# Performance work log

Hardware: AMD Instinct MI355X
Metric: run time of the kernel (lower is better)

The kernel has to match this reference:

```python
import jax, jax.numpy as jnp
import numpy as np

B, H, W = 512, 36, 36
N = H * W          # 1296 oscillators
K = 8              # couplings per oscillator
EP0 = 0.1          # kura_update_rate
ANNEAL = 0.5


def setup_inputs() -> dict:
    key = jax.random.key(0)
    k = jax.random.split(key, 8)
    return {
        "input": jax.random.normal(k[0], (B, H, W), jnp.float32),
        "initial_phase": jax.random.uniform(k[1], (B, N), jnp.float32) * (2.0 * np.pi),
        "connectivity": jax.random.randint(k[2], (B, N, K), 0, N),
        "episodes": 25,
        "conv1_w": jax.random.normal(k[3], (8, 1, 3, 3), jnp.float32) * 0.1,
        "conv1_b": jnp.zeros((8,), jnp.float32),
        "conv2_w": jax.random.normal(k[4], (16, 8, 3, 3), jnp.float32) * 0.1,
        "conv2_b": jnp.zeros((16,), jnp.float32),
        "conv3_w": jax.random.normal(k[5], (32, 16, 3, 3), jnp.float32) * 0.1,
        "conv3_b": jnp.zeros((32,), jnp.float32),
        "fc_w": jax.random.normal(k[6], (108 * 8, 108 * 32), jnp.float32) * 0.02,
        "fc_b": jnp.zeros((108 * 8,), jnp.float32),
    }


def _conv3x3(x, w, b):
    y = jax.lax.conv_general_dilated(
        x, w, (1, 1), "SAME", dimension_numbers=("NCHW", "OIHW", "NCHW"))
    return y + b[None, :, None, None]


def _kuramoto(initial_phase, coupling, connectivity, steps, ep0):
    # phase: [B,N]; coupling: [B,N,K]; connectivity: [B,N,K] neighbor indices
    gather = jax.vmap(lambda p, c: p[c])  # -> [B,N,K] neighbor phases

    def step(carry, i):
        phase, ep = carry
        neigh = gather(phase, connectivity)
        # d(phase_i) = ep * sum_j coupling_ij * sin(phase_j - phase_i)
        delta = ep * (coupling * jnp.sin(neigh - phase[:, :, None])).sum(-1)
        phase = phase + delta
        ep = ep - ANNEAL * i * ep / steps  # annealed update rate
        return (phase, ep), phase

    (_, _), phases = jax.lax.scan(
        step, (initial_phase, jnp.float32(ep0)),
        jnp.arange(steps, dtype=jnp.float32))
    # record=True: trajectory includes the initial phase
    return jnp.concatenate([initial_phase[None], phases], axis=0)  # [steps+1,B,N]


def reference(input, initial_phase, connectivity, episodes,
              conv1_w, conv1_b, conv2_w, conv2_b, conv3_w, conv3_b, fc_w, fc_b):
    x = input.reshape(-1, 1, 36, 36)
    c1 = jax.nn.relu(_conv3x3(x, conv1_w, conv1_b))
    c2 = jax.nn.relu(_conv3x3(c1, conv2_w, conv2_b))
    c3 = jax.nn.sigmoid(_conv3x3(c2, conv3_w, conv3_b))
    fc = (c3.reshape(-1, 108 * 32) @ fc_w.T + fc_b).reshape(-1, N, K)  # [B,1296,8]
    phase_list = _kuramoto(initial_phase, fc, connectivity, episodes, EP0)
    return phase_list, fc
```

## Files before the change

kernel.cpp:

```cpp
#include <hip/hip_runtime.h>
#include <hip/hip_bf16.h>

#define NPOS 1296
#define BATCH 512
#define STEPS 25
#define PH_STRIDE (BATCH * NPOS)
#define PH_TOTAL ((STEPS + 1) * PH_STRIDE)
#define FC_K 3456
#define FC_N 864
#define FC_NPAD 896
#define FC_M 6144

typedef float f32x4 __attribute__((ext_vector_type(4)));
typedef __bf16 bf16x8 __attribute__((ext_vector_type(8)));

__device__ __forceinline__ ushort f2bf(float f) {
  union { float f; unsigned u; } v; v.f = f;
  unsigned r = v.u + 0x7FFFu + ((v.u >> 16) & 1u);
  return (ushort)(r >> 16);
}
__device__ __forceinline__ float bf2f(ushort h) {
  union { unsigned u; float f; } v; v.u = ((unsigned)h) << 16; return v.f;
}

__device__ __forceinline__ void async_copy16(void* lds, const void* g) {
  __builtin_amdgcn_global_load_lds(
      (const __attribute__((address_space(1))) unsigned*)g,
      (__attribute__((address_space(3))) unsigned*)lds, 16, 0, 0);
}

__global__ __launch_bounds__(256) void wprep_kernel(
    const float* __restrict__ w1, const float* __restrict__ w2, const float* __restrict__ w3,
    float* __restrict__ w1t, ushort* __restrict__ w2t, ushort* __restrict__ w3t) {
  const int tid = threadIdx.x;
  for (int i = tid; i < 72; i += 256) {
    const int s = i / 8, co = i - s * 8;
    w1t[i] = w1[co * 9 + s];
  }
  for (int i = tid; i < 16 * 96; i += 256) {
    const int co = i / 96, k = i - co * 96;
    const int s = k / 8, ci = k - s * 8;
    w2t[i] = (k < 72) ? f2bf(w2[(co * 8 + ci) * 9 + s]) : (ushort)0;
  }
  for (int i = tid; i < 32 * 160; i += 256) {
    const int co = i / 160, k = i - co * 160;
    const int s = k / 16, ci = k - s * 16;
    w3t[i] = (k < 144) ? f2bf(w3[(co * 16 + ci) * 9 + s]) : (ushort)0;
  }
}

__global__ __launch_bounds__(256, 4) void conv_fused_kernel(
    const float* __restrict__ in, const float* __restrict__ w1t, const float* __restrict__ b1,
    const ushort* __restrict__ w2t, const float* __restrict__ b2,
    const ushort* __restrict__ w3t, const float* __restrict__ b3,
    ushort* __restrict__ aout) {
  __shared__ __align__(16) float sIn[18][40];
  __shared__ __align__(16) ushort sC1[18][40][8];
  __shared__ __align__(16) ushort sC2[16][40][16];
  const int b = blockIdx.x, band = blockIdx.y, tid = threadIdx.x;
  const int r0 = band * 12;
  const int wave = tid >> 6, lane = tid & 63;
  const int quad = lane >> 4, l16 = lane & 15;
  {
    const uint4 zz = make_uint4(0, 0, 0, 0);
    for (int i = tid; i < 180; i += 256) ((uint4*)sIn)[i] = zz;
    for (int i = tid; i < 720; i += 256) ((uint4*)sC1)[i] = zz;
    for (int i = tid; i < 1280; i += 256) ((uint4*)sC2)[i] = zz;
  }
  __syncthreads();
  for (int i = tid; i < 18 * 18; i += 256) {
    const int r = i / 18, c = i - r * 18;
    const int gy = r0 - 3 + r;
    if ((unsigned)gy < 36u)
      *(float2*)&sIn[r][2 + 2 * c] = *(const float2*)(in + (size_t)b * NPOS + gy * 36 + 2 * c);
  }
  __syncthreads();
  for (int i = tid; i < 16 * 36; i += 256) {
    const int lr = i / 36, x = i - lr * 36;
    float acc[8];
#pragma unroll
    for (int co = 0; co < 8; ++co) acc[co] = b1[co];
#pragma unroll
    for (int s = 0; s < 9; ++s) {
      const int dy = s / 3, dx = s - 3 * dy;
      const float v = sIn[lr + dy][x + 1 + dx];
#pragma unroll
      for (int co = 0; co < 8; ++co) acc[co] = fmaf(w1t[s * 8 + co], v, acc[co]);
    }
    const int g1 = r0 - 2 + lr;
    if ((unsigned)g1 < 36u) {
      uint4 pk;
      pk.x = (uint)f2bf(fmaxf(acc[0], 0.f)) | ((uint)f2bf(fmaxf(acc[1], 0.f)) << 16);
      pk.y = (uint)f2bf(fmaxf(acc[2], 0.f)) | ((uint)f2bf(fmaxf(acc[3], 0.f)) << 16);
      pk.z = (uint)f2bf(fmaxf(acc[4], 0.f)) | ((uint)f2bf(fmaxf(acc[5], 0.f)) << 16);
      pk.w = (uint)f2bf(fmaxf(acc[6], 0.f)) | ((uint)f2bf(fmaxf(acc[7], 0.f)) << 16);
      *(uint4*)&sC1[lr][x + 2][0] = pk;
    }
  }
  __syncthreads();
  bf16x8 w2f[3];
#pragma unroll
  for (int f = 0; f < 3; ++f)
    w2f[f] = *(const bf16x8*)(w2t + l16 * 96 + f * 32 + quad * 8);
  const float bias2 = b2[l16];
  for (int chunk = wave; chunk < 32; chunk += 4) {
    const int m = chunk * 16 + l16;
    const int oy = m / 36, x = m - oy * 36;
    f32x4 acc = {0.f, 0.f, 0.f, 0.f};
#pragma unroll
    for (int f = 0; f < 3; ++f) {
      const int s0 = 4 * f + quad;
      const int dy = s0 / 3, dx = s0 - 3 * dy;
      const bf16x8 af = *(const bf16x8*)&sC1[oy + dy][x + 1 + dx][0];
      acc = __builtin_amdgcn_mfma_f32_16x16x32_bf16(af, w2f[f], acc, 0, 0, 0);
    }
#pragma unroll
    for (int r = 0; r < 4; ++r) {
      const int px = chunk * 16 + quad * 4 + r;
      const int oy2 = px / 36, x2 = px - oy2 * 36;
      const int g2 = r0 - 1 + oy2;
      if (px < 504 && (unsigned)g2 < 36u)
        sC2[oy2][x2 + 2][l16] = f2bf(fmaxf(acc[r] + bias2, 0.f));
    }
  }
  __syncthreads();
  bf16x8 w3f[2][5];
#pragma unroll
  for (int t = 0; t < 2; ++t)
#pragma unroll
    for (int f = 0; f < 5; ++f)
      w3f[t][f] = *(const bf16x8*)(w3t + (t * 16 + l16) * 160 + f * 32 + quad * 8);
  const float bias3a = b3[l16], bias3b = b3[16 + l16];
  ushort* ob = aout + (size_t)b * (32 * NPOS) + r0 * 36;
  for (int chunk = wave; chunk < 27; chunk += 4) {
    const int m = chunk * 16 + l16;
    const int oy = m / 36, x = m - oy * 36;
    f32x4 acc0 = {0.f, 0.f, 0.f, 0.f}, acc1 = {0.f, 0.f, 0.f, 0.f};
#pragma unroll
    for (int f = 0; f < 5; ++f) {
      const int s0 = 2 * f + (quad >> 1);
      const int dy = s0 / 3, dx = s0 - 3 * dy;
      const bf16x8 af = *(const bf16x8*)&sC2[oy + dy][x + 1 + dx][(quad & 1) * 8];
      acc0 = __builtin_amdgcn_mfma_f32_16x16x32_bf16(af, w3f[0][f], acc0, 0, 0, 0);
      acc1 = __builtin_amdgcn_mfma_f32_16x16x32_bf16(af, w3f[1][f], acc1, 0, 0, 0);
    }
    const int pxb = chunk * 16 + quad * 4;
    ushort4 pk;
#pragma unroll
    for (int r = 0; r < 4; ++r)
      ((ushort*)&pk)[r] = f2bf(1.f / (1.f + __expf(-(acc0[r] + bias3a))));
    *(ushort4*)(ob + (size_t)l16 * NPOS + pxb) = pk;
#pragma unroll
    for (int r = 0; r < 4; ++r)
      ((ushort*)&pk)[r] = f2bf(1.f / (1.f + __expf(-(acc1[r] + bias3b))));
    *(ushort4*)(ob + (size_t)(16 + l16) * NPOS + pxb) = pk;
  }
}

__global__ __launch_bounds__(256) void wcvt_kernel(const float* __restrict__ w, ushort* __restrict__ wb) {
  const int idx = blockIdx.x * 256 + threadIdx.x;
  if (idx >= FC_NPAD * FC_K) return;
  const int n = idx / FC_K;
  wb[idx] = (n < FC_N) ? f2bf(w[idx]) : (ushort)0;
}

__global__ __launch_bounds__(256) void gemm_kernel(
    const ushort* __restrict__ A, const ushort* __restrict__ Bt,
    const float* __restrict__ bias, float* __restrict__ C) {
  __shared__ __align__(16) ushort sA[64 * 32];
  __shared__ __align__(16) ushort sB[128 * 32];
  const int tid = threadIdx.x;
  const int bn = blockIdx.x, bm = blockIdx.y;
  const int row0 = bm * 64, col0 = bn * 128;
  const int wave = tid >> 6, lane = tid & 63;
  const int wr = (wave >> 1) * 32, wc = (wave & 1) * 64;
  const int quad = lane >> 4, l16 = lane & 15;
  const int srow = tid >> 2;
  const int skk = (tid & 3) * 8;
  f32x4 acc[2][4] = {};
  const ushort* Abase = A + ((size_t)row0 + srow) * FC_K + skk;
  const ushort* Bbase = Bt + ((size_t)col0 + srow) * FC_K + skk;
  ushort* sAw = sA + wave * 512;
  ushort* sBw = sB + wave * 512;
  for (int kt = 0; kt < FC_K / 32; ++kt) {
    const int k0 = kt * 32;
    __syncthreads();
    async_copy16(sAw, Abase + k0);
    async_copy16(sBw, Bbase + k0);
    async_copy16(sBw + 2048, Bbase + (size_t)64 * FC_K + k0);
    __syncthreads();
    bf16x8 af[2], bfr[4];
#pragma unroll
    for (int t = 0; t < 2; ++t)
      af[t] = *(const bf16x8*)(sA + (wr + t * 16 + l16) * 32 + quad * 8);
#pragma unroll
    for (int t = 0; t < 4; ++t)
      bfr[t] = *(const bf16x8*)(sB + (wc + t * 16 + l16) * 32 + quad * 8);
#pragma unroll
    for (int tm = 0; tm < 2; ++tm)
#pragma unroll
      for (int tn = 0; tn < 4; ++tn)
        acc[tm][tn] = __builtin_amdgcn_mfma_f32_16x16x32_bf16(af[tm], bfr[tn], acc[tm][tn], 0, 0, 0);
  }
#pragma unroll
  for (int tn = 0; tn < 4; ++tn) {
    const int col = col0 + wc + tn * 16 + l16;
    if (col < FC_N) {
      const float bv = bias[col];
#pragma unroll
      for (int tm = 0; tm < 2; ++tm) {
#pragma unroll
        for (int r = 0; r < 4; ++r) {
          const int row = row0 + wr + tm * 16 + quad * 4 + r;
          C[(size_t)row * FC_N + col] = acc[tm][tn][r] + bv;
        }
      }
    }
  }
}

__global__ __launch_bounds__(512) void kuramoto_kernel(
    const float* __restrict__ ph0, const int* __restrict__ conn,
    const float* __restrict__ cpl, float* __restrict__ out) {
  __shared__ float ph[NPOS];
  __shared__ float2 sc[NPOS];
  const int b = blockIdx.x, tid = threadIdx.x;
  int rj[3][8];
  float rc[3][8];
#pragma unroll
  for (int s = 0; s < 3; ++s) {
    const int i = tid + s * 512;
    if (i < NPOS) {
      const float p = ph0[(size_t)b * NPOS + i];
      ph[i] = p;
      out[(size_t)b * NPOS + i] = p;
      const size_t base = (size_t)b * (NPOS * 8) + (size_t)i * 8;
      const int4 j0 = *(const int4*)(conn + base);
      const int4 j1 = *(const int4*)(conn + base + 4);
      const float4 c0 = *(const float4*)(cpl + base);
      const float4 c1 = *(const float4*)(cpl + base + 4);
      rj[s][0] = j0.x; rj[s][1] = j0.y; rj[s][2] = j0.z; rj[s][3] = j0.w;
      rj[s][4] = j1.x; rj[s][5] = j1.y; rj[s][6] = j1.z; rj[s][7] = j1.w;
      rc[s][0] = c0.x; rc[s][1] = c0.y; rc[s][2] = c0.z; rc[s][3] = c0.w;
      rc[s][4] = c1.x; rc[s][5] = c1.y; rc[s][6] = c1.z; rc[s][7] = c1.w;
    } else {
#pragma unroll
      for (int k = 0; k < 8; ++k) { rj[s][k] = 0; rc[s][k] = 0.f; }
    }
  }
  float ep = 0.1f;
  for (int t = 0; t < STEPS; ++t) {
    __syncthreads();
    for (int i = tid; i < NPOS; i += 512) {
      float s, c;
      __sincosf(ph[i], &s, &c);
      sc[i] = make_float2(s, c);
    }
    __syncthreads();
    float* op = out + (size_t)(t + 1) * PH_STRIDE + (size_t)b * NPOS;
#pragma unroll
    for (int s = 0; s < 3; ++s) {
      const int i = tid + s * 512;
      if (i < NPOS) {
        float ss = 0.f, cs = 0.f;
#pragma unroll
        for (int k = 0; k < 8; ++k) {
          const float2 v = sc[rj[s][k]];
          ss = fmaf(rc[s][k], v.x, ss);
          cs = fmaf(rc[s][k], v.y, cs);
        }
        const float2 me = sc[i];
        const float np = ph[i] + ep * (me.y * ss - me.x * cs);
        ph[i] = np;
        op[i] = np;
      }
    }
    ep = ep * (1.0f - 0.02f * (float)t);
  }
}

extern "C" void kernel_launch(void* const* d_in, const int* in_sizes, int n_in,
                              void* d_out, int out_size, void* d_ws, size_t ws_size,
                              hipStream_t stream) {
  const float* input = (const float*)d_in[0];
  const float* ph0   = (const float*)d_in[1];
  const int*   conn  = (const int*)d_in[2];
  const float* w1 = (const float*)d_in[4];
  const float* b1 = (const float*)d_in[5];
  const float* w2 = (const float*)d_in[6];
  const float* b2 = (const float*)d_in[7];
  const float* w3 = (const float*)d_in[8];
  const float* b3 = (const float*)d_in[9];
  const float* fcw = (const float*)d_in[10];
  const float* fcb = (const float*)d_in[11];
  float* out = (float*)d_out;

  ushort* Abuf = (ushort*)d_ws;
  ushort* Wbuf = (ushort*)((char*)d_ws + 42467328);
  float*  w1t  = (float*)((char*)d_ws + 48660480);
  ushort* w2t  = (ushort*)((char*)d_ws + 48660768);
  ushort* w3t  = (ushort*)((char*)d_ws + 48663840);
  float* fcout = out + PH_TOTAL;

  wprep_kernel<<<1, 256, 0, stream>>>(w1, w2, w3, w1t, w2t, w3t);
  wcvt_kernel<<<(FC_NPAD * FC_K) / 256, 256, 0, stream>>>(fcw, Wbuf);
  conv_fused_kernel<<<dim3(BATCH, 3), 256, 0, stream>>>(input, w1t, b1, w2t, b2, w3t, b3, Abuf);
  gemm_kernel<<<dim3(FC_NPAD / 128, FC_M / 64), 256, 0, stream>>>(Abuf, Wbuf, fcb, fcout);
  kuramoto_kernel<<<BATCH, 512, 0, stream>>>(ph0, conn, fcout, out);
}
```

Before: 286.9 us.

## Deepen GEMM K-step, remap blocks across XCDs, use nontemporal phase stores

The GEMM now loads two 32-wide K slices per barrier pair, which halves the number of syncs. It also uses a 1D grid whose block index is remapped so that the M tiles sharing an XCD reuse the same B columns in that die's L2. The Kuramoto kernel writes its phase trajectory with nontemporal stores, so the large streaming output does not pollute the cache. These changes add LDS usage, and the hard-coded 672-block mapping assumes 8 XCDs and 7 N-tiles.

```diff
diff --git a/kernel.cpp b/kernel.cpp
--- a/kernel.cpp
+++ b/kernel.cpp
@@ -167,10 +167,13 @@
 __global__ __launch_bounds__(256) void gemm_kernel(
     const ushort* __restrict__ A, const ushort* __restrict__ Bt,
     const float* __restrict__ bias, float* __restrict__ C) {
-  __shared__ __align__(16) ushort sA[64 * 32];
-  __shared__ __align__(16) ushort sB[128 * 32];
+  __shared__ __align__(16) ushort sA[2][64 * 32];
+  __shared__ __align__(16) ushort sB[2][128 * 32];
   const int tid = threadIdx.x;
-  const int bn = blockIdx.x, bm = blockIdx.y;
+  const int lin = blockIdx.x;
+  const int xcd = lin & 7, idx = lin >> 3;
+  const int bm = xcd + 8 * (idx / 7);
+  const int bn = idx % 7;
   const int row0 = bm * 64, col0 = bn * 128;
   const int wave = tid >> 6, lane = tid & 63;
   const int wr = (wave >> 1) * 32, wc = (wave & 1) * 64;
@@ -180,27 +183,35 @@
   f32x4 acc[2][4] = {};
   const ushort* Abase = A + ((size_t)row0 + srow) * FC_K + skk;
   const ushort* Bbase = Bt + ((size_t)col0 + srow) * FC_K + skk;
-  ushort* sAw = sA + wave * 512;
-  ushort* sBw = sB + wave * 512;
-  for (int kt = 0; kt < FC_K / 32; ++kt) {
-    const int k0 = kt * 32;
+  ushort* sA0 = sA[0] + wave * 512;
+  ushort* sA1 = sA[1] + wave * 512;
+  ushort* sB0 = sB[0] + wave * 512;
+  ushort* sB1 = sB[1] + wave * 512;
+  for (int kt = 0; kt < FC_K / 64; ++kt) {
+    const int k0 = kt * 64;
     __syncthreads();
-    async_copy16(sAw, Abase + k0);
-    async_copy16(sBw, Bbase + k0);
-    async_copy16(sBw + 2048, Bbase + (size_t)64 * FC_K + k0);
+    async_copy16(sA0, Abase + k0);
+    async_copy16(sB0, Bbase + k0);
+    async_copy16(sB0 + 2048, Bbase + (size_t)64 * FC_K + k0);
+    async_copy16(sA1, Abase + k0 + 32);
+    async_copy16(sB1, Bbase + k0 + 32);
+    async_copy16(sB1 + 2048, Bbase + (size_t)64 * FC_K + k0 + 32);
     __syncthreads();
-    bf16x8 af[2], bfr[4];
-#pragma unroll
-    for (int t = 0; t < 2; ++t)
-      af[t] = *(const bf16x8*)(sA + (wr + t * 16 + l16) * 32 + quad * 8);
-#pragma unroll
-    for (int t = 0; t < 4; ++t)
-      bfr[t] = *(const bf16x8*)(sB + (wc + t * 16 + l16) * 32 + quad * 8);
-#pragma unroll
-    for (int tm = 0; tm < 2; ++tm)
-#pragma unroll
-      for (int tn = 0; tn < 4; ++tn)
-        acc[tm][tn] = __builtin_amdgcn_mfma_f32_16x16x32_bf16(af[tm], bfr[tn], acc[tm][tn], 0, 0, 0);
+#pragma unroll
+    for (int s = 0; s < 2; ++s) {
+      bf16x8 af[2], bfr[4];
+#pragma unroll
+      for (int t = 0; t < 2; ++t)
+        af[t] = *(const bf16x8*)(sA[s] + (wr + t * 16 + l16) * 32 + quad * 8);
+#pragma unroll
+      for (int t = 0; t < 4; ++t)
+        bfr[t] = *(const bf16x8*)(sB[s] + (wc + t * 16 + l16) * 32 + quad * 8);
+#pragma unroll
+      for (int tm = 0; tm < 2; ++tm)
+#pragma unroll
+        for (int tn = 0; tn < 4; ++tn)
+          acc[tm][tn] = __builtin_amdgcn_mfma_f32_16x16x32_bf16(af[tm], bfr[tn], acc[tm][tn], 0, 0, 0);
+    }
   }
 #pragma unroll
   for (int tn = 0; tn < 4; ++tn) {
@@ -233,7 +244,7 @@
     if (i < NPOS) {
       const float p = ph0[(size_t)b * NPOS + i];
       ph[i] = p;
-      out[(size_t)b * NPOS + i] = p;
+      __builtin_nontemporal_store(p, out + (size_t)b * NPOS + i);
       const size_t base = (size_t)b * (NPOS * 8) + (size_t)i * 8;
       const int4 j0 = *(const int4*)(conn + base);
       const int4 j1 = *(const int4*)(conn + base + 4);
@@ -272,7 +283,7 @@
         const float2 me = sc[i];
         const float np = ph[i] + ep * (me.y * ss - me.x * cs);
         ph[i] = np;
-        op[i] = np;
+        __builtin_nontemporal_store(np, op + i);
       }
     }
     ep = ep * (1.0f - 0.02f * (float)t);
@@ -305,6 +316,6 @@
   wprep_kernel<<<1, 256, 0, stream>>>(w1, w2, w3, w1t, w2t, w3t);
   wcvt_kernel<<<(FC_NPAD * FC_K) / 256, 256, 0, stream>>>(fcw, Wbuf);
   conv_fused_kernel<<<dim3(BATCH, 3), 256, 0, stream>>>(input, w1t, b1, w2t, b2, w3t, b3, Abuf);
-  gemm_kernel<<<dim3(FC_NPAD / 128, FC_M / 64), 256, 0, stream>>>(Abuf, Wbuf, fcb, fcout);
+  gemm_kernel<<<672, 256, 0, stream>>>(Abuf, Wbuf, fcb, fcout);
   kuramoto_kernel<<<BATCH, 512, 0, stream>>>(ph0, conn, fcout, out);
 }
```

Result: faster. 271.0 us (-5.6%).
